# Kernel tuning notes

Hardware: AMD Instinct MI355X
Metric: run time of the kernel (lower is better)

## Reference

```python
import jax, jax.numpy as jnp
import numpy as np

IN_F = 4096
OUT_F = 11008
N_CLUSTERS = 16
TOPK = int(IN_F * 0.25)  # 1024


def setup_inputs() -> dict:
    key = jax.random.key(0)
    k1, k2, k3, k4 = jax.random.split(key, 4)
    x = jax.random.normal(k1, (1, 1, IN_F), jnp.float32)
    weight_full = jax.random.normal(k2, (OUT_F, IN_F), jnp.float32) * 0.02
    bias_full = jax.random.normal(k3, (OUT_F,), jnp.float32) * 0.02
    # cluster centers live in softmax-activation space (compared via cdist to a softmax)
    cluster_centers = jax.nn.softmax(
        jax.random.normal(k4, (N_CLUSTERS, IN_F), jnp.float32), axis=-1)
    return {"x": x, "weight_full": weight_full, "bias_full": bias_full,
            "cluster_centers": cluster_centers}


def reference(x, weight_full, bias_full, cluster_centers):
    # hot path: bsz * seq == 1
    x_flat = x.reshape(-1, x.shape[-1])                 # [1, in]
    x_avg = jnp.abs(jnp.mean(x_flat, axis=0))           # [in]
    activation = jax.nn.softmax(x_avg, axis=0)          # [in]
    # nearest cluster center (squared L2 has same argmin as L2)
    d2 = jnp.sum((cluster_centers - activation[None, :]) ** 2, axis=-1)  # [n_clusters]
    ci = jnp.argmin(d2)
    center = cluster_centers[ci]                        # [in]
    # per-cluster precomputed top-k column indices: argsort(center, descending)[:topk]
    _, topk_idx = jax.lax.top_k(center, TOPK)           # [topk]
    x_sel = jnp.take(x_flat, topk_idx, axis=1)          # [1, topk]
    w_sel = jnp.take(weight_full, topk_idx, axis=1)     # [out, topk]
    out = x_sel @ w_sel.T + bias_full                   # [1, out]
    return out.reshape(1, 1, -1)
```

## Files before the change

kernel.cpp:

```cpp
#include <hip/hip_runtime.h>

#define IN_F 4096
#define OUT_F 11008
#define NCLUST 16
#define TOPK 1024
#define NT 1024
#define NW 16
#define ROWS_PB 43

__device__ __forceinline__ float dot4(float4 a, float4 b) {
    return a.x * b.x + a.y * b.y + a.z * b.z + a.w * b.w;
}
__device__ __forceinline__ float wredsum(float v) {
    for (int o = 32; o > 0; o >>= 1) v += __shfl_down(v, o, 64);
    return v;
}

__global__ __launch_bounds__(NT) void select_mask_kernel(
    const float* __restrict__ x,
    const float* __restrict__ centers,
    float* __restrict__ xm)
{
    const int tid  = threadIdx.x;
    const int lane = tid & 63;
    const int wid  = tid >> 6;

    __shared__ __align__(16) float sact[IN_F];
    __shared__ unsigned int hist[NW * 256];
    __shared__ float swred[NW];
    __shared__ float sdot[NCLUST], scsq[NCLUST];
    __shared__ unsigned int wtot4[4], weq[NW];
    __shared__ unsigned int sprefix, sKrem, sG;
    __shared__ int sci;

    if (tid == 0) { sprefix = 0u; sKrem = TOPK; sG = 0u; }

    float4 xv = reinterpret_cast<const float4*>(x)[tid];
    float e0 = expf(fabsf(xv.x)), e1 = expf(fabsf(xv.y));
    float e2 = expf(fabsf(xv.z)), e3 = expf(fabsf(xv.w));
    reinterpret_cast<float4*>(sact)[tid] = make_float4(e0, e1, e2, e3);
    {
        float s = wredsum(e0 + e1 + e2 + e3);
        if (lane == 0) swred[wid] = s;
        hist[tid] = 0u; hist[tid + 1024] = 0u;
        hist[tid + 2048] = 0u; hist[tid + 3072] = 0u;
    }
    __syncthreads();
    float S = 0.0f;
    #pragma unroll
    for (int k = 0; k < NW; ++k) S += swred[k];

    {
        const float4* cp = reinterpret_cast<const float4*>(centers + (size_t)wid * IN_F);
        const float4* a4 = reinterpret_cast<const float4*>(sact);
        float dt = 0.0f, cq = 0.0f;
        #pragma unroll
        for (int j = 0; j < 16; ++j) {
            float4 c = cp[j * 64 + lane];
            float4 a = a4[j * 64 + lane];
            dt += dot4(c, a);
            cq += dot4(c, c);
        }
        dt = wredsum(dt);
        cq = wredsum(cq);
        if (lane == 0) { sdot[wid] = dt; scsq[wid] = cq; }
    }
    __syncthreads();

    if (wid == 0) {
        float v = (lane < NCLUST) ? (scsq[lane] - (2.0f / S) * sdot[lane]) : 3.0e38f;
        int bi = lane;
        for (int off = 8; off > 0; off >>= 1) {
            float ov = __shfl_down(v, off, 64);
            int   oi = __shfl_down(bi, off, 64);
            if (ov < v) { v = ov; bi = oi; }
        }
        if (lane == 0) sci = bi;
    }
    __syncthreads();

    unsigned int cv[4];
    {
        float4 c = reinterpret_cast<const float4*>(centers + (size_t)sci * IN_F)[tid];
        cv[0] = __float_as_uint(c.x); cv[1] = __float_as_uint(c.y);
        cv[2] = __float_as_uint(c.z); cv[3] = __float_as_uint(c.w);
    }

    for (int pass = 0; pass < 4; ++pass) {
        const int shift = 24 - 8 * pass;
        const unsigned int pfx  = sprefix;
        const unsigned int krem = sKrem;
        unsigned int* hp = &hist[wid * 256];
        #pragma unroll
        for (int j = 0; j < 4; ++j) {
            unsigned int u = cv[j];
            bool cand = (pass == 0) || ((u >> (shift + 8)) == pfx);
            if (cand) atomicAdd(&hp[(u >> shift) & 255u], 1u);
        }
        __syncthreads();
        unsigned int h = 0, s = 0;
        if (tid < 256) {
            #pragma unroll
            for (int w = 0; w < NW; ++w) { h += hist[w * 256 + tid]; hist[w * 256 + tid] = 0u; }
            s = h;
            for (int off = 1; off < 64; off <<= 1) {
                unsigned int v2 = __shfl_down(s, off, 64);
                if (lane + off < 64) s += v2;
            }
            if (lane == 0) wtot4[wid] = s;
        }
        __syncthreads();
        if (tid < 256) {
            unsigned int add = 0;
            #pragma unroll
            for (int w2 = 0; w2 < 4; ++w2) if (w2 > wid) add += wtot4[w2];
            unsigned int incl = s + add;
            unsigned int excl = incl - h;
            if (excl < krem && krem <= incl) {
                sprefix = (pfx << 8) | (unsigned int)tid;
                sKrem   = krem - excl;
            }
        }
        __syncthreads();
    }
    const unsigned int T = sprefix;

    unsigned int gt = 0, eq = 0;
    #pragma unroll
    for (int j = 0; j < 4; ++j) {
        gt += (cv[j] > T) ? 1u : 0u;
        eq += (cv[j] == T) ? 1u : 0u;
    }
    {
        unsigned int g = wredsum(0.0f) * 0.0f + gt;
    }
    {
        unsigned int g = gt;
        for (int o = 32; o > 0; o >>= 1) g += __shfl_down(g, o, 64);
        if (lane == 0) atomicAdd(&sG, g);
    }
    unsigned int p = eq;
    for (int off = 1; off < 64; off <<= 1) {
        unsigned int v2 = __shfl_up(p, off, 64);
        if (lane >= off) p += v2;
    }
    if (lane == 63) weq[wid] = p;
    __syncthreads();
    unsigned int base = p - eq;
    #pragma unroll
    for (int w = 0; w < NW; ++w) if (w < wid) base += weq[w];
    const unsigned int needEq = TOPK - sG;

    {
        unsigned int r = 0;
        float4 o;
        o.x = ((cv[0] > T) || ((cv[0] == T) && (base + r < needEq))) ? xv.x : 0.0f; r += (cv[0] == T);
        o.y = ((cv[1] > T) || ((cv[1] == T) && (base + r < needEq))) ? xv.y : 0.0f; r += (cv[1] == T);
        o.z = ((cv[2] > T) || ((cv[2] == T) && (base + r < needEq))) ? xv.z : 0.0f; r += (cv[2] == T);
        o.w = ((cv[3] > T) || ((cv[3] == T) && (base + r < needEq))) ? xv.w : 0.0f;
        reinterpret_cast<float4*>(xm)[tid] = o;
    }
}

__global__ __launch_bounds__(NT, 4) void matvec_kernel(
    const float* __restrict__ W,
    const float* __restrict__ xm,
    const float* __restrict__ bias,
    float* __restrict__ out)
{
    const int tid  = threadIdx.x;
    const int lane = tid & 63;
    const int wid  = tid >> 6;
    const int rbase = blockIdx.x * ROWS_PB;

    float4 sl[16];
    {
        const float4* xm4 = reinterpret_cast<const float4*>(xm);
        #pragma unroll
        for (int j = 0; j < 16; ++j) sl[j] = xm4[j * 64 + lane];
    }

    for (int r = wid; r < ROWS_PB; r += NW) {
        const int row = rbase + r;
        const float4* wr = reinterpret_cast<const float4*>(W + (size_t)row * IN_F);
        float acc = 0.0f;
        #pragma unroll
        for (int j = 0; j < 16; ++j) {
            acc += dot4(wr[j * 64 + lane], sl[j]);
        }
        acc = wredsum(acc);
        if (lane == 0) out[row] = acc + bias[row];
    }
}

extern "C" void kernel_launch(void* const* d_in, const int* in_sizes, int n_in,
                              void* d_out, int out_size, void* d_ws, size_t ws_size,
                              hipStream_t stream) {
    const float* x       = (const float*)d_in[0];
    const float* weight  = (const float*)d_in[1];
    const float* bias    = (const float*)d_in[2];
    const float* centers = (const float*)d_in[3];
    float* out = (float*)d_out;
    float* xm  = (float*)d_ws;

    select_mask_kernel<<<1, NT, 0, stream>>>(x, centers, xm);
    matvec_kernel<<<256, NT, 0, stream>>>(weight, xm, bias, out);
}
```

Baseline: 45.40 us.

## Split each matvec row across the whole block with shared-memory partial reduction

Result: faster. 43.42 us, median of 2 (-4.4%).

```diff
diff --git a/kernel.cpp b/kernel.cpp
--- a/kernel.cpp
+++ b/kernel.cpp
@@ -8,8 +8,10 @@
 #define NW 16
 #define ROWS_PB 43
 
-__device__ __forceinline__ float dot4(float4 a, float4 b) {
-    return a.x * b.x + a.y * b.y + a.z * b.z + a.w * b.w;
+typedef float f4 __attribute__((ext_vector_type(4)));
+
+__device__ __forceinline__ float dotf4(f4 a, f4 b) {
+    return a[0] * b[0] + a[1] * b[1] + a[2] * b[2] + a[3] * b[3];
 }
 __device__ __forceinline__ float wredsum(float v) {
     for (int o = 32; o > 0; o >>= 1) v += __shfl_down(v, o, 64);
@@ -58,8 +60,8 @@
         for (int j = 0; j < 16; ++j) {
             float4 c = cp[j * 64 + lane];
             float4 a = a4[j * 64 + lane];
-            dt += dot4(c, a);
-            cq += dot4(c, c);
+            dt += c.x * a.x + c.y * a.y + c.z * a.z + c.w * a.w;
+            cq += c.x * c.x + c.y * c.y + c.z * c.z + c.w * c.w;
         }
         dt = wredsum(dt);
         cq = wredsum(cq);
@@ -132,9 +134,6 @@
         eq += (cv[j] == T) ? 1u : 0u;
     }
     {
-        unsigned int g = wredsum(0.0f) * 0.0f + gt;
-    }
-    {
         unsigned int g = gt;
         for (int o = 32; o > 0; o >>= 1) g += __shfl_down(g, o, 64);
         if (lane == 0) atomicAdd(&sG, g);
@@ -162,7 +161,7 @@
     }
 }
 
-__global__ __launch_bounds__(NT, 4) void matvec_kernel(
+__global__ __launch_bounds__(NT) void matvec_kernel(
     const float* __restrict__ W,
     const float* __restrict__ xm,
     const float* __restrict__ bias,
@@ -173,23 +172,49 @@
     const int wid  = tid >> 6;
     const int rbase = blockIdx.x * ROWS_PB;
 
-    float4 sl[16];
-    {
-        const float4* xm4 = reinterpret_cast<const float4*>(xm);
-        #pragma unroll
-        for (int j = 0; j < 16; ++j) sl[j] = xm4[j * 64 + lane];
-    }
-
-    for (int r = wid; r < ROWS_PB; r += NW) {
-        const int row = rbase + r;
-        const float4* wr = reinterpret_cast<const float4*>(W + (size_t)row * IN_F);
-        float acc = 0.0f;
-        #pragma unroll
-        for (int j = 0; j < 16; ++j) {
-            acc += dot4(wr[j * 64 + lane], sl[j]);
-        }
-        acc = wredsum(acc);
-        if (lane == 0) out[row] = acc + bias[row];
+    __shared__ float spart[ROWS_PB][NW + 1];
+
+    const f4 xv = ((const f4*)xm)[tid];
+    const f4* wp = (const f4*)(W + (size_t)rbase * IN_F);
+
+    int r = 0;
+    #pragma unroll 2
+    for (; r + 4 <= ROWS_PB; r += 4) {
+        f4 wa = wp[(size_t)(r + 0) * 1024 + tid];
+        f4 wb = wp[(size_t)(r + 1) * 1024 + tid];
+        f4 wc = wp[(size_t)(r + 2) * 1024 + tid];
+        f4 wd = wp[(size_t)(r + 3) * 1024 + tid];
+        float pa = dotf4(wa, xv);
+        float pb = dotf4(wb, xv);
+        float pc = dotf4(wc, xv);
+        float pd = dotf4(wd, xv);
+        #pragma unroll
+        for (int o = 32; o > 0; o >>= 1) {
+            pa += __shfl_down(pa, o, 64);
+            pb += __shfl_down(pb, o, 64);
+            pc += __shfl_down(pc, o, 64);
+            pd += __shfl_down(pd, o, 64);
+        }
+        if (lane == 0) {
+            spart[r + 0][wid] = pa;
+            spart[r + 1][wid] = pb;
+            spart[r + 2][wid] = pc;
+            spart[r + 3][wid] = pd;
+        }
+    }
+    for (; r < ROWS_PB; ++r) {
+        f4 w = wp[(size_t)r * 1024 + tid];
+        float p = wredsum(dotf4(w, xv));
+        if (lane == 0) spart[r][wid] = p;
+    }
+    __syncthreads();
+
+    if (tid < ROWS_PB) {
+        float s = 0.0f;
+        #pragma unroll
+        for (int w = 0; w < NW; ++w) s += spart[tid][w];
+        const int row = rbase + tid;
+        out[row] = s + bias[row];
     }
 }
 
```
